# Optimization experiments

Measured on AMD Instinct MI355X. Metric: run time of the kernel, lower is better.

## Reference

```python
import jax, jax.numpy as jnp
import numpy as np

N, D_IN, D_H, D_ATT, N_CLUSTERS, N_CLASSES = 20000, 1024, 512, 256, 10, 4


def setup_inputs() -> dict:
    key = jax.random.key(0)
    ks = jax.random.split(key, 20)
    s = 0.02
    inp = {
        "x_path": jax.random.normal(ks[0], (N, D_IN), dtype=jnp.float32),
        "cluster_id": jax.random.randint(ks[1], (N,), 0, N_CLUSTERS, dtype=jnp.int64 if jax.config.jax_enable_x64 else jnp.int32),
        # per-cluster expert MLPs (phi_i): 1024->512->512
        "W1": jax.random.normal(ks[2], (N_CLUSTERS, D_IN, D_H), dtype=jnp.float32) * s,
        "b1": jnp.zeros((N_CLUSTERS, D_H), dtype=jnp.float32),
        "W2": jax.random.normal(ks[3], (N_CLUSTERS, D_H, D_H), dtype=jnp.float32) * s,
        "b2": jnp.zeros((N_CLUSTERS, D_H), dtype=jnp.float32),
        # attention_net: fc (512->512) then gated attention (L=512, D=256, 1)
        "Wfc": jax.random.normal(ks[4], (D_H, D_H), dtype=jnp.float32) * s,
        "bfc": jnp.zeros((D_H,), dtype=jnp.float32),
        "Wa": jax.random.normal(ks[5], (D_H, D_ATT), dtype=jnp.float32) * s,
        "ba": jnp.zeros((D_ATT,), dtype=jnp.float32),
        "Wb": jax.random.normal(ks[6], (D_H, D_ATT), dtype=jnp.float32) * s,
        "bb": jnp.zeros((D_ATT,), dtype=jnp.float32),
        "Wc": jax.random.normal(ks[7], (D_ATT, 1), dtype=jnp.float32) * s,
        "bc": jnp.zeros((1,), dtype=jnp.float32),
        # rho: 512->256
        "Wrho": jax.random.normal(ks[8], (D_H, D_ATT), dtype=jnp.float32) * s,
        "brho": jnp.zeros((D_ATT,), dtype=jnp.float32),
        # classifier: 256->4
        "Wcls": jax.random.normal(ks[9], (D_ATT, N_CLASSES), dtype=jnp.float32) * s,
        "bcls": jnp.zeros((N_CLASSES,), dtype=jnp.float32),
    }
    return inp


def reference(x_path, cluster_id, W1, b1, W2, b2, Wfc, bfc, Wa, ba, Wb, bb, Wc, bc, Wrho, brho, Wcls, bcls):
    C = W1.shape[0]
    # dispatch mask [N, C]; per-cluster counts
    onehot = jax.nn.one_hot(cluster_id, C, dtype=x_path.dtype)
    counts = jnp.maximum(onehot.sum(axis=0), 1.0)  # [C]
    # per-cluster expert MLP + masked mean-pool (AdaptiveAvgPool1d(1) over instances)
    pooled = []
    for i in range(C):  # small static loop over experts
        h = jax.nn.relu(x_path @ W1[i] + b1[i])      # [N, 512]
        h = jax.nn.relu(h @ W2[i] + b2[i])           # [N, 512]
        pooled.append((onehot[:, i] @ h) / counts[i])  # masked mean -> [512]
    h_cluster = jnp.stack(pooled, axis=0)            # [C, 512]
    # attention_net: fc then gated attention
    h = jax.nn.relu(h_cluster @ Wfc + bfc)           # [C, 512]
    a = jnp.tanh(h @ Wa + ba)                        # [C, 256]
    b = jax.nn.sigmoid(h @ Wb + bb)                  # [C, 256]
    A = ((a * b) @ Wc + bc).T                        # [1, C]
    A = jax.nn.softmax(A, axis=1)
    h_path = A @ h                                   # [1, 512]
    h_path = jax.nn.relu(h_path @ Wrho + brho).squeeze()  # [256]
    logits = (h_path @ Wcls + bcls)[None, :]         # [1, 4]
    Y_hat = jnp.argmax(logits, axis=1, keepdims=True)
    hazards = jax.nn.sigmoid(logits)
    S = jnp.cumprod(1.0 - hazards, axis=1)
    return hazards, S, Y_hat
```

## Files before the change

kernel.cpp:

```cpp
#include <hip/hip_runtime.h>
#include <hip/hip_bf16.h>
#include <math.h>


#define C_NUM 10
#define D_IN 1024
#define D_H 512
#define D_ATT 256
#define N_CLS 4
#define BM 128
#define BN 128
#define BKS 64

typedef __attribute__((ext_vector_type(8))) short short8v;
typedef __attribute__((ext_vector_type(4))) short short4v;
typedef __attribute__((ext_vector_type(4))) float f32x4;

__device__ __forceinline__ short f2bf(float f) {
    __hip_bfloat16 h = __float2bfloat16(f);
    return *reinterpret_cast<short*>(&h);
}

__device__ __forceinline__ void gload_lds16(const void* g, void* l) {
    __builtin_amdgcn_global_load_lds((const __attribute__((address_space(1))) unsigned int*)g,
                                     (__attribute__((address_space(3))) unsigned int*)l,
                                     16, 0, 0);
}

__device__ __forceinline__ int xcd_swizzle(int orig, int nwg) {
    int q = nwg >> 3, r = nwg & 7;
    int xcd = orig & 7, base = orig >> 3;
    return (xcd < r ? xcd * (q + 1) : r * (q + 1) + (xcd - r) * q) + base;
}

__global__ __launch_bounds__(256) void k_hist(const int* __restrict__ cid, int* counts, int n) {
    __shared__ int lc[C_NUM];
    int tid = threadIdx.x;
    if (tid < C_NUM) lc[tid] = 0;
    __syncthreads();
    int i = blockIdx.x * 256 + tid;
    if (i < n) atomicAdd(&lc[cid[i]], 1);
    __syncthreads();
    if (tid < C_NUM && lc[tid] > 0) atomicAdd(&counts[tid], lc[tid]);
}

__global__ void k_offsets(const int* __restrict__ counts, int* aoff) {
    if (threadIdx.x == 0) {
        int off = 0;
        for (int c = 0; c < C_NUM; ++c) {
            aoff[c] = off;
            off += ((counts[c] + BM - 1) / BM) * BM;
        }
        aoff[C_NUM] = off;
    }
}

__global__ __launch_bounds__(256) void k_scatter(const int* __restrict__ cid, int* cursor,
                                                 const int* __restrict__ aoff, int* bucket, int n) {
    __shared__ int lc[C_NUM];
    __shared__ int base[C_NUM];
    int tid = threadIdx.x;
    if (tid < C_NUM) lc[tid] = 0;
    __syncthreads();
    int i = blockIdx.x * 256 + tid;
    int c = 0, lpos = 0;
    bool valid = (i < n);
    if (valid) { c = cid[i]; lpos = atomicAdd(&lc[c], 1); }
    __syncthreads();
    if (tid < C_NUM) base[tid] = (lc[tid] > 0) ? atomicAdd(&cursor[tid], lc[tid]) : 0;
    __syncthreads();
    if (valid) bucket[aoff[c] + base[c] + lpos] = i;
}

__global__ __launch_bounds__(256) void k_convert(const float* __restrict__ x,
                                                 const int* __restrict__ bucket,
                                                 short* __restrict__ xb) {
    int tid = threadIdx.x;
    int row = blockIdx.x * 2 + (tid >> 7);
    int e0 = (tid & 127) * 8;
    int r = bucket[row];
    f32x4 f0 = {0.f, 0.f, 0.f, 0.f}, f1 = {0.f, 0.f, 0.f, 0.f};
    if (r >= 0) {
        const f32x4* p = (const f32x4*)&x[(size_t)r * D_IN + e0];
        f0 = p[0]; f1 = p[1];
    }
    short8v v;
#pragma unroll
    for (int e = 0; e < 4; ++e) { v[e] = f2bf(f0[e]); v[4 + e] = f2bf(f1[e]); }
    *(short8v*)&xb[(size_t)row * D_IN + e0] = v;
}

__global__ __launch_bounds__(256) void k_transpose(const float* __restrict__ W,
                                                   short* __restrict__ Wt, int K, int N) {
    __shared__ float t[64][65];
    int k0 = blockIdx.x * 64, n0 = blockIdx.y * 64, cc = blockIdx.z;
    const float* src = W + (size_t)cc * K * N;
    short* dst = Wt + (size_t)cc * N * K;
    int tid = threadIdx.x;
    int tk = tid >> 4, tn4 = (tid & 15) * 4;
#pragma unroll
    for (int it = 0; it < 4; ++it) {
        int k = tk + it * 16;
        f32x4 v = *(const f32x4*)&src[(size_t)(k0 + k) * N + n0 + tn4];
        t[k][tn4 + 0] = v[0]; t[k][tn4 + 1] = v[1];
        t[k][tn4 + 2] = v[2]; t[k][tn4 + 3] = v[3];
    }
    __syncthreads();
    int wn = tid >> 2, kq = (tid & 3) * 16;
#pragma unroll
    for (int q = 0; q < 4; ++q) {
        int k = kq + q * 4;
        short4v o;
#pragma unroll
        for (int e = 0; e < 4; ++e) o[e] = f2bf(t[k + e][wn]);
        *(short4v*)&dst[(size_t)(n0 + wn) * K + k0 + k] = o;
    }
}

__global__ __launch_bounds__(256) void k_gemm1b(
    const short* __restrict__ xb, const short* __restrict__ Wt, const float* __restrict__ b1,
    const int* __restrict__ bucket, const int* __restrict__ aoff, short* __restrict__ h1)
{
    __shared__ short As[BM * BKS];
    __shared__ short Bs[BN * BKS];
    __shared__ int ridx[BM];

    int wg = xcd_swizzle(blockIdx.x, gridDim.x);
    int rowStart = (wg >> 2) * BM;
    if (rowStart >= aoff[C_NUM]) return;
    int c = 0;
    while (c < C_NUM - 1 && rowStart >= aoff[c + 1]) ++c;
    int colStart = (wg & 3) * BN;

    int tid = threadIdx.x;
    int lane = tid & 63;
    int wid = tid >> 6;
    int wm = wid >> 1, wn = wid & 1;

    if (tid < BM) ridx[tid] = bucket[rowStart + tid];

    int l8 = lane >> 3;
    int sslot = (lane & 7) ^ l8;
    const short* abase = xb + (size_t)(rowStart + l8) * D_IN + sslot * 8;
    const short* bbase = Wt + ((size_t)c * D_H + colStart + l8) * D_IN + sslot * 8;

    f32x4 acc[4][4];
#pragma unroll
    for (int i = 0; i < 4; ++i)
#pragma unroll
        for (int j = 0; j < 4; ++j)
            acc[i][j] = f32x4{0.f, 0.f, 0.f, 0.f};

    for (int k0 = 0; k0 < D_IN; k0 += BKS) {
#pragma unroll
        for (int q = 0; q < 4; ++q) {
            int rb = (q * 4 + wid) * 8;
            gload_lds16(abase + (size_t)rb * D_IN + k0, &As[rb * BKS]);
            gload_lds16(bbase + (size_t)rb * D_IN + k0, &Bs[rb * BKS]);
        }
        __syncthreads();
#pragma unroll
        for (int kk = 0; kk < 2; ++kk) {
            short8v af[4], bfr[4];
#pragma unroll
            for (int i = 0; i < 4; ++i) {
                int row = wm * 64 + i * 16 + (lane & 15);
                int slot = (kk * 4 + (lane >> 4)) ^ (row & 7);
                af[i] = *(const short8v*)&As[row * BKS + slot * 8];
            }
#pragma unroll
            for (int j = 0; j < 4; ++j) {
                int nn = wn * 64 + j * 16 + (lane & 15);
                int slot = (kk * 4 + (lane >> 4)) ^ (nn & 7);
                bfr[j] = *(const short8v*)&Bs[nn * BKS + slot * 8];
            }
#pragma unroll
            for (int i = 0; i < 4; ++i)
#pragma unroll
                for (int j = 0; j < 4; ++j)
                    acc[i][j] = __builtin_amdgcn_mfma_f32_16x16x32_bf16(af[i], bfr[j], acc[i][j], 0, 0, 0);
        }
        __syncthreads();
    }

    const float* bias = b1 + c * D_H;
    float bj[4];
#pragma unroll
    for (int j = 0; j < 4; ++j) bj[j] = bias[colStart + wn * 64 + j * 16 + (lane & 15)];
#pragma unroll
    for (int i = 0; i < 4; ++i) {
#pragma unroll
        for (int r = 0; r < 4; ++r) {
            int rowl = wm * 64 + i * 16 + (lane >> 4) * 4 + r;
            bool valid = (ridx[rowl] >= 0);
            size_t gro = (size_t)(rowStart + rowl) * D_H + colStart + wn * 64 + (lane & 15);
#pragma unroll
            for (int j = 0; j < 4; ++j) {
                float v = valid ? fmaxf(acc[i][j][r] + bj[j], 0.f) : 0.f;
                h1[gro + j * 16] = f2bf(v);
            }
        }
    }
}

__global__ __launch_bounds__(256) void k_gemm1_mfma(
    const float* __restrict__ x, const short* __restrict__ Wt, const float* __restrict__ b1,
    const int* __restrict__ bucket, const int* __restrict__ aoff, short* __restrict__ h1)
{
    __shared__ short As[BM * BKS];
    __shared__ short Bs[BN * BKS];
    __shared__ int ridx[BM];

    int rowStart = blockIdx.x * BM;
    if (rowStart >= aoff[C_NUM]) return;
    int c = 0;
    while (c < C_NUM - 1 && rowStart >= aoff[c + 1]) ++c;
    int colStart = blockIdx.y * BN;

    int tid = threadIdx.x;
    int lane = tid & 63;
    int wid = tid >> 6;
    int wm = wid >> 1, wn = wid & 1;

    if (tid < BM) ridx[tid] = bucket[rowStart + tid];
    __syncthreads();

    int arow = tid >> 1;
    int khalf = tid & 1;
    int agr = ridx[arow];
    const float* aptr = x + (size_t)(agr < 0 ? 0 : agr) * D_IN + khalf * 32;

    int l8 = lane >> 3;
    int sslot = (lane & 7) ^ l8;
    const short* bbase = Wt + ((size_t)c * D_H + colStart + l8) * D_IN + sslot * 8;

    f32x4 acc[4][4];
#pragma unroll
    for (int i = 0; i < 4; ++i)
#pragma unroll
        for (int j = 0; j < 4; ++j)
            acc[i][j] = f32x4{0.f, 0.f, 0.f, 0.f};

    for (int k0 = 0; k0 < D_IN; k0 += BKS) {
#pragma unroll
        for (int q = 0; q < 4; ++q) {
            int nbase = (q * 4 + wid) * 8;
            gload_lds16(bbase + (size_t)nbase * D_IN + k0, &Bs[nbase * BKS]);
        }
        {
            const f32x4* p = (const f32x4*)(aptr + k0);
#pragma unroll
            for (int q = 0; q < 4; ++q) {
                f32x4 f0 = {0.f, 0.f, 0.f, 0.f}, f1 = {0.f, 0.f, 0.f, 0.f};
                if (agr >= 0) { f0 = p[2 * q]; f1 = p[2 * q + 1]; }
                short8v v;
#pragma unroll
                for (int e = 0; e < 4; ++e) { v[e] = f2bf(f0[e]); v[4 + e] = f2bf(f1[e]); }
                int slot = (khalf * 4 + q) ^ (arow & 7);
                *(short8v*)&As[arow * BKS + slot * 8] = v;
            }
        }
        __syncthreads();
#pragma unroll
        for (int kk = 0; kk < 2; ++kk) {
            short8v af[4], bfr[4];
#pragma unroll
            for (int i = 0; i < 4; ++i) {
                int row = wm * 64 + i * 16 + (lane & 15);
                int slot = (kk * 4 + (lane >> 4)) ^ (row & 7);
                af[i] = *(const short8v*)&As[row * BKS + slot * 8];
            }
#pragma unroll
            for (int j = 0; j < 4; ++j) {
                int nn = wn * 64 + j * 16 + (lane & 15);
                int slot = (kk * 4 + (lane >> 4)) ^ (nn & 7);
                bfr[j] = *(const short8v*)&Bs[nn * BKS + slot * 8];
            }
#pragma unroll
            for (int i = 0; i < 4; ++i)
#pragma unroll
                for (int j = 0; j < 4; ++j)
                    acc[i][j] = __builtin_amdgcn_mfma_f32_16x16x32_bf16(af[i], bfr[j], acc[i][j], 0, 0, 0);
        }
        __syncthreads();
    }

    const float* bias = b1 + c * D_H;
    float bj[4];
#pragma unroll
    for (int j = 0; j < 4; ++j) bj[j] = bias[colStart + wn * 64 + j * 16 + (lane & 15)];
#pragma unroll
    for (int i = 0; i < 4; ++i) {
#pragma unroll
        for (int r = 0; r < 4; ++r) {
            int rowl = wm * 64 + i * 16 + (lane >> 4) * 4 + r;
            bool valid = (ridx[rowl] >= 0);
            size_t gro = (size_t)(rowStart + rowl) * D_H + colStart + wn * 64 + (lane & 15);
#pragma unroll
            for (int j = 0; j < 4; ++j) {
                float v = valid ? fmaxf(acc[i][j][r] + bj[j], 0.f) : 0.f;
                h1[gro + j * 16] = f2bf(v);
            }
        }
    }
}

__global__ __launch_bounds__(256) void k_gemm2_mfma(
    const short* __restrict__ h1, const short* __restrict__ Wt, const float* __restrict__ b2,
    const int* __restrict__ bucket, const int* __restrict__ aoff, float* __restrict__ pooled)
{
    __shared__ short As[BM * BKS];
    __shared__ short Bs[BN * BKS];
    __shared__ int ridx[BM];

    int wg = xcd_swizzle(blockIdx.x, gridDim.x);
    int rowStart = (wg >> 2) * BM;
    if (rowStart >= aoff[C_NUM]) return;
    int c = 0;
    while (c < C_NUM - 1 && rowStart >= aoff[c + 1]) ++c;
    int colStart = (wg & 3) * BN;

    int tid = threadIdx.x;
    int lane = tid & 63;
    int wid = tid >> 6;
    int wm = wid >> 1, wn = wid & 1;

    if (tid < BM) ridx[tid] = bucket[rowStart + tid];

    int l8 = lane >> 3;
    int sslot = (lane & 7) ^ l8;
    const short* abase = h1 + (size_t)(rowStart + l8) * D_H + sslot * 8;
    const short* bbase = Wt + ((size_t)c * D_H + colStart + l8) * D_H + sslot * 8;

    f32x4 acc[4][4];
#pragma unroll
    for (int i = 0; i < 4; ++i)
#pragma unroll
        for (int j = 0; j < 4; ++j)
            acc[i][j] = f32x4{0.f, 0.f, 0.f, 0.f};

    for (int k0 = 0; k0 < D_H; k0 += BKS) {
#pragma unroll
        for (int q = 0; q < 4; ++q) {
            int rb = (q * 4 + wid) * 8;
            gload_lds16(abase + (size_t)rb * D_H + k0, &As[rb * BKS]);
            gload_lds16(bbase + (size_t)rb * D_H + k0, &Bs[rb * BKS]);
        }
        __syncthreads();
#pragma unroll
        for (int kk = 0; kk < 2; ++kk) {
            short8v af[4], bfr[4];
#pragma unroll
            for (int i = 0; i < 4; ++i) {
                int row = wm * 64 + i * 16 + (lane & 15);
                int slot = (kk * 4 + (lane >> 4)) ^ (row & 7);
                af[i] = *(const short8v*)&As[row * BKS + slot * 8];
            }
#pragma unroll
            for (int j = 0; j < 4; ++j) {
                int nn = wn * 64 + j * 16 + (lane & 15);
                int slot = (kk * 4 + (lane >> 4)) ^ (nn & 7);
                bfr[j] = *(const short8v*)&Bs[nn * BKS + slot * 8];
            }
#pragma unroll
            for (int i = 0; i < 4; ++i)
#pragma unroll
                for (int j = 0; j < 4; ++j)
                    acc[i][j] = __builtin_amdgcn_mfma_f32_16x16x32_bf16(af[i], bfr[j], acc[i][j], 0, 0, 0);
        }
        __syncthreads();
    }

    const float* bias = b2 + c * D_H;
    float bj[4];
#pragma unroll
    for (int j = 0; j < 4; ++j) bj[j] = bias[colStart + wn * 64 + j * 16 + (lane & 15)];
    float csum[4] = {0.f, 0.f, 0.f, 0.f};
#pragma unroll
    for (int i = 0; i < 4; ++i) {
#pragma unroll
        for (int r = 0; r < 4; ++r) {
            int rowl = wm * 64 + i * 16 + (lane >> 4) * 4 + r;
            float m = (ridx[rowl] >= 0) ? 1.f : 0.f;
#pragma unroll
            for (int j = 0; j < 4; ++j)
                csum[j] += m * fmaxf(acc[i][j][r] + bj[j], 0.f);
        }
    }
#pragma unroll
    for (int j = 0; j < 4; ++j) {
        float s = csum[j];
        s += __shfl_xor(s, 16, 64);
        s += __shfl_xor(s, 32, 64);
        if ((lane >> 4) == 0)
            atomicAdd(&pooled[c * D_H + colStart + wn * 64 + j * 16 + lane], s);
    }
}

__global__ __launch_bounds__(256) void k_tA(
    const float* __restrict__ pooled, const int* __restrict__ counts,
    const float* __restrict__ Wfc, const float* __restrict__ bfc,
    float* __restrict__ hfc)
{
    __shared__ float hcs[C_NUM][D_H];
    __shared__ float red[4][64][C_NUM];
    int tid = threadIdx.x;
    for (int idx = tid; idx < C_NUM * D_H; idx += 256) {
        int cc = idx >> 9;
        hcs[cc][idx & (D_H - 1)] = pooled[idx] / fmaxf((float)counts[cc], 1.f);
    }
    __syncthreads();
    int col = blockIdx.x * 64 + (tid & 63);
    int kq = tid >> 6, k0 = kq * 128;
    float acc[C_NUM] = {};
    for (int k = 0; k < 128; ++k) {
        float wv = Wfc[(size_t)(k0 + k) * D_H + col];
#pragma unroll
        for (int cc = 0; cc < C_NUM; ++cc) acc[cc] += hcs[cc][k0 + k] * wv;
    }
#pragma unroll
    for (int cc = 0; cc < C_NUM; ++cc) red[kq][tid & 63][cc] = acc[cc];
    __syncthreads();
    if (kq == 0) {
        float bv = bfc[col];
#pragma unroll
        for (int cc = 0; cc < C_NUM; ++cc) {
            float s = red[0][tid][cc] + red[1][tid][cc] + red[2][tid][cc] + red[3][tid][cc];
            hfc[cc * D_H + col] = fmaxf(s + bv, 0.f);
        }
    }
}

__global__ __launch_bounds__(256) void k_tB(
    const float* __restrict__ hfc,
    const float* __restrict__ Wa, const float* __restrict__ ba,
    const float* __restrict__ Wb, const float* __restrict__ bb,
    const float* __restrict__ Wc,
    float* __restrict__ scores)
{
    __shared__ float hfs[C_NUM][D_H];
    __shared__ float red[4][64][C_NUM][2];
    int tid = threadIdx.x;
    for (int idx = tid; idx < C_NUM * D_H; idx += 256) {
        hfs[idx >> 9][idx & (D_H - 1)] = hfc[idx];
    }
    __syncthreads();
    int ad = blockIdx.x * 64 + (tid & 63);
    int kq = tid >> 6, k0 = kq * 128;
    float sa[C_NUM] = {}, sb[C_NUM] = {};
    for (int k = 0; k < 128; ++k) {
        float wav = Wa[(size_t)(k0 + k) * D_ATT + ad];
        float wbv = Wb[(size_t)(k0 + k) * D_ATT + ad];
#pragma unroll
        for (int cc = 0; cc < C_NUM; ++cc) {
            float h = hfs[cc][k0 + k];
            sa[cc] += h * wav;
            sb[cc] += h * wbv;
        }
    }
#pragma unroll
    for (int cc = 0; cc < C_NUM; ++cc) {
        red[kq][tid & 63][cc][0] = sa[cc];
        red[kq][tid & 63][cc][1] = sb[cc];
    }
    __syncthreads();
    if (kq == 0) {
        float bav = ba[ad], bbv = bb[ad], wcv = Wc[ad];
#pragma unroll
        for (int cc = 0; cc < C_NUM; ++cc) {
            float sat = red[0][tid][cc][0] + red[1][tid][cc][0] + red[2][tid][cc][0] + red[3][tid][cc][0];
            float sbt = red[0][tid][cc][1] + red[1][tid][cc][1] + red[2][tid][cc][1] + red[3][tid][cc][1];
            float v = tanhf(sat + bav) * (1.f / (1.f + expf(-(sbt + bbv)))) * wcv;
            v += __shfl_xor(v, 1, 64); v += __shfl_xor(v, 2, 64); v += __shfl_xor(v, 4, 64);
            v += __shfl_xor(v, 8, 64); v += __shfl_xor(v, 16, 64); v += __shfl_xor(v, 32, 64);
            if (tid == 0) atomicAdd(&scores[cc], v);
        }
    }
}

__global__ __launch_bounds__(512) void k_tC(
    const float* __restrict__ scores, const float* __restrict__ bc,
    const float* __restrict__ hfc, float* __restrict__ hp)
{
    __shared__ float sA[C_NUM];
    int tid = threadIdx.x;
    if (tid == 0) {
        float sc2[C_NUM];
        float mx = -1e30f;
#pragma unroll
        for (int cc = 0; cc < C_NUM; ++cc) { sc2[cc] = scores[cc] + bc[0]; mx = fmaxf(mx, sc2[cc]); }
        float sum = 0.f;
#pragma unroll
        for (int cc = 0; cc < C_NUM; ++cc) { sc2[cc] = expf(sc2[cc] - mx); sum += sc2[cc]; }
#pragma unroll
        for (int cc = 0; cc < C_NUM; ++cc) sA[cc] = sc2[cc] / sum;
    }
    __syncthreads();
    float s = 0.f;
#pragma unroll
    for (int cc = 0; cc < C_NUM; ++cc) s += sA[cc] * hfc[cc * D_H + tid];
    hp[tid] = s;
}

__global__ __launch_bounds__(256) void k_tD(
    const float* __restrict__ hp, const float* __restrict__ Wrho,
    float* __restrict__ hr_raw)
{
    __shared__ float hps[128];
    int tid = threadIdx.x;
    int k0 = blockIdx.x * 128;
    if (tid < 128) hps[tid] = hp[k0 + tid];
    __syncthreads();
    float acc = 0.f;
    for (int k = 0; k < 128; ++k)
        acc += hps[k] * Wrho[(size_t)(k0 + k) * D_ATT + tid];
    atomicAdd(&hr_raw[tid], acc);
}

__global__ __launch_bounds__(256) void k_tE(
    const float* __restrict__ hr_raw, const float* __restrict__ brho,
    const float* __restrict__ Wcls, const float* __restrict__ bcls,
    float* __restrict__ out)
{
    __shared__ float cpart[4][N_CLS];
    int tid = threadIdx.x, lane = tid & 63, w = tid >> 6;
    float h = fmaxf(hr_raw[tid] + brho[tid], 0.f);
    f32x4 wv = *(const f32x4*)&Wcls[tid * N_CLS];
    float v[N_CLS];
#pragma unroll
    for (int l = 0; l < N_CLS; ++l) {
        v[l] = h * wv[l];
        v[l] += __shfl_xor(v[l], 1, 64); v[l] += __shfl_xor(v[l], 2, 64);
        v[l] += __shfl_xor(v[l], 4, 64); v[l] += __shfl_xor(v[l], 8, 64);
        v[l] += __shfl_xor(v[l], 16, 64); v[l] += __shfl_xor(v[l], 32, 64);
    }
    if (lane == 0) {
#pragma unroll
        for (int l = 0; l < N_CLS; ++l) cpart[w][l] = v[l];
    }
    __syncthreads();
    if (tid == 0) {
        float lg[N_CLS];
#pragma unroll
        for (int l = 0; l < N_CLS; ++l)
            lg[l] = cpart[0][l] + cpart[1][l] + cpart[2][l] + cpart[3][l] + bcls[l];
        int best = 0;
#pragma unroll
        for (int l = 1; l < N_CLS; ++l) if (lg[l] > lg[best]) best = l;
        float Sv = 1.f;
#pragma unroll
        for (int l = 0; l < N_CLS; ++l) {
            float hz = 1.f / (1.f + expf(-lg[l]));
            out[l] = hz;
            Sv *= (1.f - hz);
            out[4 + l] = Sv;
        }
        out[8] = (float)best;
    }
}

extern "C" void kernel_launch(void* const* d_in, const int* in_sizes, int n_in,
                              void* d_out, int out_size, void* d_ws, size_t ws_size,
                              hipStream_t stream)
{
    const float* x    = (const float*)d_in[0];
    const int*   cid  = (const int*)d_in[1];
    const float* W1   = (const float*)d_in[2];
    const float* b1   = (const float*)d_in[3];
    const float* W2   = (const float*)d_in[4];
    const float* b2   = (const float*)d_in[5];
    const float* Wfc  = (const float*)d_in[6];
    const float* bfc  = (const float*)d_in[7];
    const float* Wa   = (const float*)d_in[8];
    const float* ba   = (const float*)d_in[9];
    const float* Wb   = (const float*)d_in[10];
    const float* bb   = (const float*)d_in[11];
    const float* Wc   = (const float*)d_in[12];
    const float* bc   = (const float*)d_in[13];
    const float* Wrho = (const float*)d_in[14];
    const float* brho = (const float*)d_in[15];
    const float* Wcls = (const float*)d_in[16];
    const float* bcls = (const float*)d_in[17];
    float* out = (float*)d_out;

    int n = in_sizes[0] / D_IN;
    int rowTiles = (n + BM - 1) / BM + C_NUM;
    int npadMax = rowTiles * BM;

    char* w = (char*)d_ws;
    int* counts   = (int*)w;
    int* cursor   = counts + 16;
    float* scores = (float*)(counts + 32);
    float* hr_raw = scores + 16;
    float* pooled = hr_raw + 256;
    size_t zero_bytes = (size_t)(16 + 16 + 16 + 256 + 5120) * 4;
    int* aoff   = (int*)(pooled + 5120);
    float* hp   = (float*)(aoff + 16);
    float* hfc  = hp + 512;
    int* bucket = (int*)(hfc + 5120);
    short* Wt1 = (short*)(bucket + npadMax);
    short* Wt2 = Wt1 + (size_t)C_NUM * D_H * D_IN;
    short* h1  = Wt2 + (size_t)C_NUM * D_H * D_H;
    short* xb  = h1 + (size_t)npadMax * D_H;
    size_t need_big = (size_t)((char*)(xb + (size_t)npadMax * D_IN) - w);
    bool big = ws_size >= need_big;

    hipMemsetAsync(w, 0, zero_bytes, stream);
    hipMemsetAsync(bucket, 0xFF, (size_t)npadMax * 4, stream);

    int nb = (n + 255) / 256;
    k_hist<<<nb, 256, 0, stream>>>(cid, counts, n);
    k_offsets<<<1, 64, 0, stream>>>(counts, aoff);
    k_scatter<<<nb, 256, 0, stream>>>(cid, cursor, aoff, bucket, n);

    k_transpose<<<dim3(D_IN / 64, D_H / 64, C_NUM), 256, 0, stream>>>(W1, Wt1, D_IN, D_H);
    k_transpose<<<dim3(D_H / 64, D_H / 64, C_NUM), 256, 0, stream>>>(W2, Wt2, D_H, D_H);

    if (big) {
        k_convert<<<npadMax / 2, 256, 0, stream>>>(x, bucket, xb);
        k_gemm1b<<<rowTiles * 4, 256, 0, stream>>>(xb, Wt1, b1, bucket, aoff, h1);
    } else {
        k_gemm1_mfma<<<dim3(rowTiles, 4), 256, 0, stream>>>(x, Wt1, b1, bucket, aoff, h1);
    }
    k_gemm2_mfma<<<rowTiles * 4, 256, 0, stream>>>(h1, Wt2, b2, bucket, aoff, pooled);

    k_tA<<<8, 256, 0, stream>>>(pooled, counts, Wfc, bfc, hfc);
    k_tB<<<4, 256, 0, stream>>>(hfc, Wa, ba, Wb, bb, Wc, scores);
    k_tC<<<1, 512, 0, stream>>>(scores, bc, hfc, hp);
    k_tD<<<4, 256, 0, stream>>>(hp, Wrho, hr_raw);
    k_tE<<<1, 256, 0, stream>>>(hr_raw, brho, Wcls, bcls, out);
}
```

Before: 146.3 us.

## Fuse fp32-to-bf16 conversion into GEMM1 and merge softmax-pool with rho matvec

Drops the separate gather/convert pass that wrote a bf16 copy of the sorted input, and uses a single GEMM1 that reads fp32 rows directly through the bucket index and converts them in-kernel, with the XCD-swizzled 1D grid. It also fuses the attention softmax/pooling kernel with the Wrho matvec into one 16-block kernel that recomputes the softmax per block. This removes one large write and reread of the bf16 activations and one kernel launch. The cost is that the fp32 gather load path in the GEMM may be less efficient than the direct-to-LDS bf16 loads.

```diff
diff --git a/kernel.cpp b/kernel.cpp
--- a/kernel.cpp
+++ b/kernel.cpp
@@ -72,24 +72,6 @@
     if (valid) bucket[aoff[c] + base[c] + lpos] = i;
 }
 
-__global__ __launch_bounds__(256) void k_convert(const float* __restrict__ x,
-                                                 const int* __restrict__ bucket,
-                                                 short* __restrict__ xb) {
-    int tid = threadIdx.x;
-    int row = blockIdx.x * 2 + (tid >> 7);
-    int e0 = (tid & 127) * 8;
-    int r = bucket[row];
-    f32x4 f0 = {0.f, 0.f, 0.f, 0.f}, f1 = {0.f, 0.f, 0.f, 0.f};
-    if (r >= 0) {
-        const f32x4* p = (const f32x4*)&x[(size_t)r * D_IN + e0];
-        f0 = p[0]; f1 = p[1];
-    }
-    short8v v;
-#pragma unroll
-    for (int e = 0; e < 4; ++e) { v[e] = f2bf(f0[e]); v[4 + e] = f2bf(f1[e]); }
-    *(short8v*)&xb[(size_t)row * D_IN + e0] = v;
-}
-
 __global__ __launch_bounds__(256) void k_transpose(const float* __restrict__ W,
                                                    short* __restrict__ Wt, int K, int N) {
     __shared__ float t[64][65];
@@ -117,8 +99,8 @@
     }
 }
 
-__global__ __launch_bounds__(256) void k_gemm1b(
-    const short* __restrict__ xb, const short* __restrict__ Wt, const float* __restrict__ b1,
+__global__ __launch_bounds__(256) void k_gemm1(
+    const float* __restrict__ x, const short* __restrict__ Wt, const float* __restrict__ b1,
     const int* __restrict__ bucket, const int* __restrict__ aoff, short* __restrict__ h1)
 {
     __shared__ short As[BM * BKS];
@@ -131,91 +113,6 @@
     int c = 0;
     while (c < C_NUM - 1 && rowStart >= aoff[c + 1]) ++c;
     int colStart = (wg & 3) * BN;
-
-    int tid = threadIdx.x;
-    int lane = tid & 63;
-    int wid = tid >> 6;
-    int wm = wid >> 1, wn = wid & 1;
-
-    if (tid < BM) ridx[tid] = bucket[rowStart + tid];
-
-    int l8 = lane >> 3;
-    int sslot = (lane & 7) ^ l8;
-    const short* abase = xb + (size_t)(rowStart + l8) * D_IN + sslot * 8;
-    const short* bbase = Wt + ((size_t)c * D_H + colStart + l8) * D_IN + sslot * 8;
-
-    f32x4 acc[4][4];
-#pragma unroll
-    for (int i = 0; i < 4; ++i)
-#pragma unroll
-        for (int j = 0; j < 4; ++j)
-            acc[i][j] = f32x4{0.f, 0.f, 0.f, 0.f};
-
-    for (int k0 = 0; k0 < D_IN; k0 += BKS) {
-#pragma unroll
-        for (int q = 0; q < 4; ++q) {
-            int rb = (q * 4 + wid) * 8;
-            gload_lds16(abase + (size_t)rb * D_IN + k0, &As[rb * BKS]);
-            gload_lds16(bbase + (size_t)rb * D_IN + k0, &Bs[rb * BKS]);
-        }
-        __syncthreads();
-#pragma unroll
-        for (int kk = 0; kk < 2; ++kk) {
-            short8v af[4], bfr[4];
-#pragma unroll
-            for (int i = 0; i < 4; ++i) {
-                int row = wm * 64 + i * 16 + (lane & 15);
-                int slot = (kk * 4 + (lane >> 4)) ^ (row & 7);
-                af[i] = *(const short8v*)&As[row * BKS + slot * 8];
-            }
-#pragma unroll
-            for (int j = 0; j < 4; ++j) {
-                int nn = wn * 64 + j * 16 + (lane & 15);
-                int slot = (kk * 4 + (lane >> 4)) ^ (nn & 7);
-                bfr[j] = *(const short8v*)&Bs[nn * BKS + slot * 8];
-            }
-#pragma unroll
-            for (int i = 0; i < 4; ++i)
-#pragma unroll
-                for (int j = 0; j < 4; ++j)
-                    acc[i][j] = __builtin_amdgcn_mfma_f32_16x16x32_bf16(af[i], bfr[j], acc[i][j], 0, 0, 0);
-        }
-        __syncthreads();
-    }
-
-    const float* bias = b1 + c * D_H;
-    float bj[4];
-#pragma unroll
-    for (int j = 0; j < 4; ++j) bj[j] = bias[colStart + wn * 64 + j * 16 + (lane & 15)];
-#pragma unroll
-    for (int i = 0; i < 4; ++i) {
-#pragma unroll
-        for (int r = 0; r < 4; ++r) {
-            int rowl = wm * 64 + i * 16 + (lane >> 4) * 4 + r;
-            bool valid = (ridx[rowl] >= 0);
-            size_t gro = (size_t)(rowStart + rowl) * D_H + colStart + wn * 64 + (lane & 15);
-#pragma unroll
-            for (int j = 0; j < 4; ++j) {
-                float v = valid ? fmaxf(acc[i][j][r] + bj[j], 0.f) : 0.f;
-                h1[gro + j * 16] = f2bf(v);
-            }
-        }
-    }
-}
-
-__global__ __launch_bounds__(256) void k_gemm1_mfma(
-    const float* __restrict__ x, const short* __restrict__ Wt, const float* __restrict__ b1,
-    const int* __restrict__ bucket, const int* __restrict__ aoff, short* __restrict__ h1)
-{
-    __shared__ short As[BM * BKS];
-    __shared__ short Bs[BN * BKS];
-    __shared__ int ridx[BM];
-
-    int rowStart = blockIdx.x * BM;
-    if (rowStart >= aoff[C_NUM]) return;
-    int c = 0;
-    while (c < C_NUM - 1 && rowStart >= aoff[c + 1]) ++c;
-    int colStart = blockIdx.y * BN;
 
     int tid = threadIdx.x;
     int lane = tid & 63;
@@ -478,13 +375,15 @@
     }
 }
 
-__global__ __launch_bounds__(512) void k_tC(
+__global__ __launch_bounds__(256) void k_tCD(
     const float* __restrict__ scores, const float* __restrict__ bc,
-    const float* __restrict__ hfc, float* __restrict__ hp)
-{
-    __shared__ float sA[C_NUM];
-    int tid = threadIdx.x;
-    if (tid == 0) {
+    const float* __restrict__ hfc, const float* __restrict__ Wrho,
+    float* __restrict__ hr_raw)
+{
+    __shared__ float hps[32];
+    int tid = threadIdx.x;
+    int k0 = blockIdx.x * 32;
+    if (tid < 32) {
         float sc2[C_NUM];
         float mx = -1e30f;
 #pragma unroll
@@ -492,27 +391,15 @@
         float sum = 0.f;
 #pragma unroll
         for (int cc = 0; cc < C_NUM; ++cc) { sc2[cc] = expf(sc2[cc] - mx); sum += sc2[cc]; }
-#pragma unroll
-        for (int cc = 0; cc < C_NUM; ++cc) sA[cc] = sc2[cc] / sum;
-    }
-    __syncthreads();
-    float s = 0.f;
-#pragma unroll
-    for (int cc = 0; cc < C_NUM; ++cc) s += sA[cc] * hfc[cc * D_H + tid];
-    hp[tid] = s;
-}
-
-__global__ __launch_bounds__(256) void k_tD(
-    const float* __restrict__ hp, const float* __restrict__ Wrho,
-    float* __restrict__ hr_raw)
-{
-    __shared__ float hps[128];
-    int tid = threadIdx.x;
-    int k0 = blockIdx.x * 128;
-    if (tid < 128) hps[tid] = hp[k0 + tid];
+        float s = 0.f;
+#pragma unroll
+        for (int cc = 0; cc < C_NUM; ++cc) s += (sc2[cc] / sum) * hfc[cc * D_H + k0 + tid];
+        hps[tid] = s;
+    }
     __syncthreads();
     float acc = 0.f;
-    for (int k = 0; k < 128; ++k)
+#pragma unroll 8
+    for (int k = 0; k < 32; ++k)
         acc += hps[k] * Wrho[(size_t)(k0 + k) * D_ATT + tid];
     atomicAdd(&hr_raw[tid], acc);
 }
@@ -595,15 +482,11 @@
     float* pooled = hr_raw + 256;
     size_t zero_bytes = (size_t)(16 + 16 + 16 + 256 + 5120) * 4;
     int* aoff   = (int*)(pooled + 5120);
-    float* hp   = (float*)(aoff + 16);
-    float* hfc  = hp + 512;
+    float* hfc  = (float*)(aoff + 16);
     int* bucket = (int*)(hfc + 5120);
     short* Wt1 = (short*)(bucket + npadMax);
     short* Wt2 = Wt1 + (size_t)C_NUM * D_H * D_IN;
     short* h1  = Wt2 + (size_t)C_NUM * D_H * D_H;
-    short* xb  = h1 + (size_t)npadMax * D_H;
-    size_t need_big = (size_t)((char*)(xb + (size_t)npadMax * D_IN) - w);
-    bool big = ws_size >= need_big;
 
     hipMemsetAsync(w, 0, zero_bytes, stream);
     hipMemsetAsync(bucket, 0xFF, (size_t)npadMax * 4, stream);
@@ -616,17 +499,11 @@
     k_transpose<<<dim3(D_IN / 64, D_H / 64, C_NUM), 256, 0, stream>>>(W1, Wt1, D_IN, D_H);
     k_transpose<<<dim3(D_H / 64, D_H / 64, C_NUM), 256, 0, stream>>>(W2, Wt2, D_H, D_H);
 
-    if (big) {
-        k_convert<<<npadMax / 2, 256, 0, stream>>>(x, bucket, xb);
-        k_gemm1b<<<rowTiles * 4, 256, 0, stream>>>(xb, Wt1, b1, bucket, aoff, h1);
-    } else {
-        k_gemm1_mfma<<<dim3(rowTiles, 4), 256, 0, stream>>>(x, Wt1, b1, bucket, aoff, h1);
-    }
+    k_gemm1<<<rowTiles * 4, 256, 0, stream>>>(x, Wt1, b1, bucket, aoff, h1);
     k_gemm2_mfma<<<rowTiles * 4, 256, 0, stream>>>(h1, Wt2, b2, bucket, aoff, pooled);
 
     k_tA<<<8, 256, 0, stream>>>(pooled, counts, Wfc, bfc, hfc);
     k_tB<<<4, 256, 0, stream>>>(hfc, Wa, ba, Wb, bb, Wc, scores);
-    k_tC<<<1, 512, 0, stream>>>(scores, bc, hfc, hp);
-    k_tD<<<4, 256, 0, stream>>>(hp, Wrho, hr_raw);
+    k_tCD<<<16, 256, 0, stream>>>(scores, bc, hfc, Wrho, hr_raw);
     k_tE<<<1, 256, 0, stream>>>(hr_raw, brho, Wcls, bcls, out);
 }
```

Measured after the change: 158.1 us. 8.0% more time.

## Fuse bucketing into one kernel, linear bf16 convert, gather rows in GEMM1

Applied to the files above, without the earlier changes.

Replaces the histogram, offset and scatter kernels and a bucket memset with a single one-block kernel that counts clusters using wave ballots, builds the offsets and writes the bucket. It also merges the two weight transposes into one launch and merges the softmax/pool step with the rho matvec. The x conversion to bf16 now runs linearly, with no gather through the bucket, and GEMM1 gathers rows through per-lane pointers into LDS. This cuts launch count and the padded convert. The risks are a serial single-block bucketing pass over 20k elements and less coalesced row gathers in GEMM1.

```diff
diff --git a/kernel.cpp b/kernel.cpp
--- a/kernel.cpp
+++ b/kernel.cpp
@@ -33,69 +33,86 @@
     return (xcd < r ? xcd * (q + 1) : r * (q + 1) + (xcd - r) * q) + base;
 }
 
-__global__ __launch_bounds__(256) void k_hist(const int* __restrict__ cid, int* counts, int n) {
+__global__ __launch_bounds__(1024) void k_bucket(const int* __restrict__ cid, int n,
+                                                 int* counts, int* aoff, int* bucket) {
     __shared__ int lc[C_NUM];
-    int tid = threadIdx.x;
+    __shared__ int lcur[C_NUM];
+    __shared__ int loff[C_NUM + 1];
+    int tid = threadIdx.x, lane = tid & 63;
     if (tid < C_NUM) lc[tid] = 0;
     __syncthreads();
-    int i = blockIdx.x * 256 + tid;
-    if (i < n) atomicAdd(&lc[cid[i]], 1);
-    __syncthreads();
-    if (tid < C_NUM && lc[tid] > 0) atomicAdd(&counts[tid], lc[tid]);
-}
-
-__global__ void k_offsets(const int* __restrict__ counts, int* aoff) {
-    if (threadIdx.x == 0) {
+    for (int i0 = 0; i0 < n; i0 += 1024) {
+        int i = i0 + tid;
+        int c = (i < n) ? cid[i] : -1;
+#pragma unroll
+        for (int cc = 0; cc < C_NUM; ++cc) {
+            unsigned long long m = __ballot(c == cc);
+            if (m != 0ull && lane == __ffsll(m) - 1)
+                atomicAdd(&lc[cc], __popcll(m));
+        }
+    }
+    __syncthreads();
+    if (tid == 0) {
         int off = 0;
         for (int c = 0; c < C_NUM; ++c) {
-            aoff[c] = off;
-            off += ((counts[c] + BM - 1) / BM) * BM;
-        }
-        aoff[C_NUM] = off;
-    }
-}
-
-__global__ __launch_bounds__(256) void k_scatter(const int* __restrict__ cid, int* cursor,
-                                                 const int* __restrict__ aoff, int* bucket, int n) {
-    __shared__ int lc[C_NUM];
-    __shared__ int base[C_NUM];
-    int tid = threadIdx.x;
-    if (tid < C_NUM) lc[tid] = 0;
-    __syncthreads();
-    int i = blockIdx.x * 256 + tid;
-    int c = 0, lpos = 0;
-    bool valid = (i < n);
-    if (valid) { c = cid[i]; lpos = atomicAdd(&lc[c], 1); }
-    __syncthreads();
-    if (tid < C_NUM) base[tid] = (lc[tid] > 0) ? atomicAdd(&cursor[tid], lc[tid]) : 0;
-    __syncthreads();
-    if (valid) bucket[aoff[c] + base[c] + lpos] = i;
-}
-
-__global__ __launch_bounds__(256) void k_convert(const float* __restrict__ x,
-                                                 const int* __restrict__ bucket,
-                                                 short* __restrict__ xb) {
-    int tid = threadIdx.x;
-    int row = blockIdx.x * 2 + (tid >> 7);
-    int e0 = (tid & 127) * 8;
-    int r = bucket[row];
-    f32x4 f0 = {0.f, 0.f, 0.f, 0.f}, f1 = {0.f, 0.f, 0.f, 0.f};
-    if (r >= 0) {
-        const f32x4* p = (const f32x4*)&x[(size_t)r * D_IN + e0];
-        f0 = p[0]; f1 = p[1];
-    }
+            loff[c] = off; lcur[c] = off;
+            off += ((lc[c] + BM - 1) / BM) * BM;
+        }
+        loff[C_NUM] = off;
+    }
+    __syncthreads();
+    if (tid < C_NUM) { counts[tid] = lc[tid]; aoff[tid] = loff[tid]; }
+    if (tid == C_NUM) aoff[C_NUM] = loff[C_NUM];
+    for (int c = 0; c < C_NUM; ++c)
+        for (int i = loff[c] + lc[c] + tid; i < loff[c + 1]; i += 1024) bucket[i] = -1;
+    for (int i0 = 0; i0 < n; i0 += 1024) {
+        int i = i0 + tid;
+        int c = (i < n) ? cid[i] : -1;
+#pragma unroll
+        for (int cc = 0; cc < C_NUM; ++cc) {
+            unsigned long long m = __ballot(c == cc);
+            if (c == cc) {
+                int leader = __ffsll(m) - 1;
+                int rank = __popcll(m & ((1ull << lane) - 1ull));
+                int base = 0;
+                if (lane == leader) base = atomicAdd(&lcur[cc], __popcll(m));
+                base = __shfl(base, leader, 64);
+                bucket[base + rank] = i;
+            }
+        }
+    }
+}
+
+__global__ __launch_bounds__(256) void k_convertlin(const float* __restrict__ x,
+                                                    short* __restrict__ xbl) {
+    size_t i = (size_t)blockIdx.x * 256 + threadIdx.x;
+    const f32x4* p = (const f32x4*)(x + i * 8);
+    f32x4 f0 = p[0], f1 = p[1];
     short8v v;
 #pragma unroll
     for (int e = 0; e < 4; ++e) { v[e] = f2bf(f0[e]); v[4 + e] = f2bf(f1[e]); }
-    *(short8v*)&xb[(size_t)row * D_IN + e0] = v;
-}
-
-__global__ __launch_bounds__(256) void k_transpose(const float* __restrict__ W,
-                                                   short* __restrict__ Wt, int K, int N) {
+    *(short8v*)&xbl[i * 8] = v;
+}
+
+__global__ __launch_bounds__(256) void k_transpose2(
+    const float* __restrict__ W1, short* __restrict__ Wt1,
+    const float* __restrict__ W2, short* __restrict__ Wt2)
+{
     __shared__ float t[64][65];
-    int k0 = blockIdx.x * 64, n0 = blockIdx.y * 64, cc = blockIdx.z;
-    const float* src = W + (size_t)cc * K * N;
-    short* dst = Wt + (size_t)cc * N * K;
+    int bid = blockIdx.x;
+    const float* src; short* dst; int K, N, k0, n0;
+    if (bid < C_NUM * 128) {
+        int cc = bid >> 7, r = bid & 127;
+        k0 = (r & 15) * 64; n0 = (r >> 4) * 64;
+        src = W1 + (size_t)cc * D_IN * D_H; dst = Wt1 + (size_t)cc * D_H * D_IN;
+        K = D_IN; N = D_H;
+    } else {
+        int idx = bid - C_NUM * 128;
+        int cc = idx >> 6, r = idx & 63;
+        k0 = (r & 7) * 64; n0 = (r >> 3) * 64;
+        src = W2 + (size_t)cc * D_H * D_H; dst = Wt2 + (size_t)cc * D_H * D_H;
+        K = D_H; N = D_H;
+    }
     int tid = threadIdx.x;
     int tk = tid >> 4, tn4 = (tid & 15) * 4;
 #pragma unroll
@@ -117,8 +134,8 @@
     }
 }
 
-__global__ __launch_bounds__(256) void k_gemm1b(
-    const short* __restrict__ xb, const short* __restrict__ Wt, const float* __restrict__ b1,
+__global__ __launch_bounds__(256) void k_gemm1g(
+    const short* __restrict__ xbl, const short* __restrict__ Wt, const float* __restrict__ b1,
     const int* __restrict__ bucket, const int* __restrict__ aoff, short* __restrict__ h1)
 {
     __shared__ short As[BM * BKS];
@@ -138,10 +155,16 @@
     int wm = wid >> 1, wn = wid & 1;
 
     if (tid < BM) ridx[tid] = bucket[rowStart + tid];
+    __syncthreads();
 
     int l8 = lane >> 3;
     int sslot = (lane & 7) ^ l8;
-    const short* abase = xb + (size_t)(rowStart + l8) * D_IN + sslot * 8;
+    const short* aq[4];
+#pragma unroll
+    for (int q = 0; q < 4; ++q) {
+        int rr = ridx[(q * 4 + wid) * 8 + l8];
+        aq[q] = xbl + (size_t)(rr < 0 ? 0 : rr) * D_IN + sslot * 8;
+    }
     const short* bbase = Wt + ((size_t)c * D_H + colStart + l8) * D_IN + sslot * 8;
 
     f32x4 acc[4][4];
@@ -155,7 +178,7 @@
 #pragma unroll
         for (int q = 0; q < 4; ++q) {
             int rb = (q * 4 + wid) * 8;
-            gload_lds16(abase + (size_t)rb * D_IN + k0, &As[rb * BKS]);
+            gload_lds16(aq[q] + k0, &As[rb * BKS]);
             gload_lds16(bbase + (size_t)rb * D_IN + k0, &Bs[rb * BKS]);
         }
         __syncthreads();
@@ -203,7 +226,7 @@
     }
 }
 
-__global__ __launch_bounds__(256) void k_gemm1_mfma(
+__global__ __launch_bounds__(256) void k_gemm1f(
     const float* __restrict__ x, const short* __restrict__ Wt, const float* __restrict__ b1,
     const int* __restrict__ bucket, const int* __restrict__ aoff, short* __restrict__ h1)
 {
@@ -478,13 +501,15 @@
     }
 }
 
-__global__ __launch_bounds__(512) void k_tC(
+__global__ __launch_bounds__(256) void k_tCD(
     const float* __restrict__ scores, const float* __restrict__ bc,
-    const float* __restrict__ hfc, float* __restrict__ hp)
-{
-    __shared__ float sA[C_NUM];
+    const float* __restrict__ hfc, const float* __restrict__ Wrho,
+    float* __restrict__ hr_raw)
+{
+    __shared__ float hps[32];
     int tid = threadIdx.x;
-    if (tid == 0) {
+    int k0 = blockIdx.x * 32;
+    if (tid < 32) {
         float sc2[C_NUM];
         float mx = -1e30f;
 #pragma unroll
@@ -492,27 +517,15 @@
         float sum = 0.f;
 #pragma unroll
         for (int cc = 0; cc < C_NUM; ++cc) { sc2[cc] = expf(sc2[cc] - mx); sum += sc2[cc]; }
-#pragma unroll
-        for (int cc = 0; cc < C_NUM; ++cc) sA[cc] = sc2[cc] / sum;
-    }
-    __syncthreads();
-    float s = 0.f;
-#pragma unroll
-    for (int cc = 0; cc < C_NUM; ++cc) s += sA[cc] * hfc[cc * D_H + tid];
-    hp[tid] = s;
-}
-
-__global__ __launch_bounds__(256) void k_tD(
-    const float* __restrict__ hp, const float* __restrict__ Wrho,
-    float* __restrict__ hr_raw)
-{
-    __shared__ float hps[128];
-    int tid = threadIdx.x;
-    int k0 = blockIdx.x * 128;
-    if (tid < 128) hps[tid] = hp[k0 + tid];
+        float s = 0.f;
+#pragma unroll
+        for (int cc = 0; cc < C_NUM; ++cc) s += (sc2[cc] / sum) * hfc[cc * D_H + k0 + tid];
+        hps[tid] = s;
+    }
     __syncthreads();
     float acc = 0.f;
-    for (int k = 0; k < 128; ++k)
+#pragma unroll 8
+    for (int k = 0; k < 32; ++k)
         acc += hps[k] * Wrho[(size_t)(k0 + k) * D_ATT + tid];
     atomicAdd(&hr_raw[tid], acc);
 }
@@ -589,44 +602,35 @@
 
     char* w = (char*)d_ws;
     int* counts   = (int*)w;
-    int* cursor   = counts + 16;
-    float* scores = (float*)(counts + 32);
+    float* scores = (float*)(counts + 16);
     float* hr_raw = scores + 16;
     float* pooled = hr_raw + 256;
-    size_t zero_bytes = (size_t)(16 + 16 + 16 + 256 + 5120) * 4;
+    size_t zero_bytes = (size_t)(16 + 16 + 256 + 5120) * 4;
     int* aoff   = (int*)(pooled + 5120);
-    float* hp   = (float*)(aoff + 16);
-    float* hfc  = hp + 512;
+    float* hfc  = (float*)(aoff + 16);
     int* bucket = (int*)(hfc + 5120);
     short* Wt1 = (short*)(bucket + npadMax);
     short* Wt2 = Wt1 + (size_t)C_NUM * D_H * D_IN;
     short* h1  = Wt2 + (size_t)C_NUM * D_H * D_H;
-    short* xb  = h1 + (size_t)npadMax * D_H;
-    size_t need_big = (size_t)((char*)(xb + (size_t)npadMax * D_IN) - w);
+    short* xbl = h1 + (size_t)npadMax * D_H;
+    size_t need_big = (size_t)((char*)(xbl + (size_t)n * D_IN) - w);
     bool big = ws_size >= need_big;
 
     hipMemsetAsync(w, 0, zero_bytes, stream);
-    hipMemsetAsync(bucket, 0xFF, (size_t)npadMax * 4, stream);
-
-    int nb = (n + 255) / 256;
-    k_hist<<<nb, 256, 0, stream>>>(cid, counts, n);
-    k_offsets<<<1, 64, 0, stream>>>(counts, aoff);
-    k_scatter<<<nb, 256, 0, stream>>>(cid, cursor, aoff, bucket, n);
-
-    k_transpose<<<dim3(D_IN / 64, D_H / 64, C_NUM), 256, 0, stream>>>(W1, Wt1, D_IN, D_H);
-    k_transpose<<<dim3(D_H / 64, D_H / 64, C_NUM), 256, 0, stream>>>(W2, Wt2, D_H, D_H);
+
+    k_bucket<<<1, 1024, 0, stream>>>(cid, n, counts, aoff, bucket);
+    k_transpose2<<<C_NUM * 128 + C_NUM * 64, 256, 0, stream>>>(W1, Wt1, W2, Wt2);
 
     if (big) {
-        k_convert<<<npadMax / 2, 256, 0, stream>>>(x, bucket, xb);
-        k_gemm1b<<<rowTiles * 4, 256, 0, stream>>>(xb, Wt1, b1, bucket, aoff, h1);
+        k_convertlin<<<(n * D_IN / 8 + 255) / 256, 256, 0, stream>>>(x, xbl);
+        k_gemm1g<<<rowTiles * 4, 256, 0, stream>>>(xbl, Wt1, b1, bucket, aoff, h1);
     } else {
-        k_gemm1_mfma<<<dim3(rowTiles, 4), 256, 0, stream>>>(x, Wt1, b1, bucket, aoff, h1);
+        k_gemm1f<<<dim3(rowTiles, 4), 256, 0, stream>>>(x, Wt1, b1, bucket, aoff, h1);
     }
     k_gemm2_mfma<<<rowTiles * 4, 256, 0, stream>>>(h1, Wt2, b2, bucket, aoff, pooled);
 
     k_tA<<<8, 256, 0, stream>>>(pooled, counts, Wfc, bfc, hfc);
     k_tB<<<4, 256, 0, stream>>>(hfc, Wa, ba, Wb, bb, Wc, scores);
-    k_tC<<<1, 512, 0, stream>>>(scores, bc, hfc, hp);
-    k_tD<<<4, 256, 0, stream>>>(hp, Wrho, hr_raw);
+    k_tCD<<<16, 256, 0, stream>>>(scores, bc, hfc, Wrho, hr_raw);
     k_tE<<<1, 256, 0, stream>>>(hr_raw, brho, Wcls, bcls, out);
 }
```

Result: slower. 203.2 us (+38.8%).
